# Kernel optimization log

Measured on AMD Instinct MI355X. Metric: run time of the kernel, lower is better.

## Reference

```python
import jax, jax.numpy as jnp
import numpy as np

N_NODES = 6000
DEG = 16
N_EDGES = N_NODES * DEG
D_MODEL = 256
D_MSG = 64
D_FF = 4 * D_MODEL
N_LAYERS = 3
N_SPECIES = 108
RBF_BINS = D_MODEL
RBF_VMIN, RBF_VMAX = 0.0, 8.0


def setup_inputs():
    key = jax.random.key(0)
    ks = jax.random.split(key, 16)
    rng = np.random.default_rng(0)
    # graph: each node i has DEG in-edges (dst block-structured), random sources
    atomic_number = jnp.asarray(rng.integers(1, N_SPECIES, N_NODES), dtype=jnp.int32)
    dst = np.repeat(np.arange(N_NODES), DEG)
    src = rng.integers(0, N_NODES, N_EDGES)
    # angle graph t: nodes = edges of g; edges = all ordered pairs of in-edges sharing dst
    pq = np.array([(p, q) for p in range(DEG) for q in range(DEG) if p != q], dtype=np.int64)
    off = (np.arange(N_NODES) * DEG)[:, None]
    t_src = (off + pq[:, 0][None, :]).reshape(-1)
    t_dst = (off + pq[:, 1][None, :]).reshape(-1)
    r = jax.random.normal(ks[0], (N_EDGES, 3), dtype=jnp.float32) * 2.0  # bond vectors, |r|~3A
    s_dm = 1.0 / np.sqrt(D_MODEL)
    s_dmsg = 1.0 / np.sqrt(D_MSG)
    s_ff = 1.0 / np.sqrt(D_FF)
    return {
        'r': r,
        'atomic_number': atomic_number,
        'src': jnp.asarray(src, dtype=jnp.int32),
        'dst': jnp.asarray(dst, dtype=jnp.int32),
        't_src': jnp.asarray(t_src, dtype=jnp.int32),
        't_dst': jnp.asarray(t_dst, dtype=jnp.int32),
        'emb': jax.random.normal(ks[1], (N_SPECIES, D_MODEL), dtype=jnp.float32),
        'Wsrc': jax.random.normal(ks[2], (N_LAYERS, D_MSG, D_MODEL), dtype=jnp.float32) * s_dm,
        'bsrc': jnp.zeros((N_LAYERS, D_MSG), jnp.float32),
        'Wdst': jax.random.normal(ks[3], (N_LAYERS, D_MSG, D_MODEL), dtype=jnp.float32) * s_dm,
        'bdst': jnp.zeros((N_LAYERS, D_MSG), jnp.float32),
        'Wedge': jax.random.normal(ks[4], (N_LAYERS, D_MSG, D_MODEL), dtype=jnp.float32) * s_dm,
        'bedge': jnp.zeros((N_LAYERS, D_MSG), jnp.float32),
        'attn': jax.random.normal(ks[5], (N_LAYERS, D_MSG), dtype=jnp.float32) * s_dmsg,
        'W1': jax.random.normal(ks[6], (N_LAYERS, D_FF, D_MSG), dtype=jnp.float32) * s_dmsg,
        'b1': jnp.zeros((N_LAYERS, D_FF), jnp.float32),
        'W2': jax.random.normal(ks[7], (N_LAYERS, D_MODEL, D_FF), dtype=jnp.float32) * s_ff,
        'b2': jnp.zeros((N_LAYERS, D_MODEL), jnp.float32),
        'Wfc': jax.random.normal(ks[8], (1, D_MODEL), dtype=jnp.float32) * s_dm,
        'bfc': jnp.zeros((1,), jnp.float32),
    }


def _segment_softmax(logits, seg, num):
    m = jax.ops.segment_max(logits, seg, num_segments=num)
    ex = jnp.exp(logits - m[seg])
    z = jax.ops.segment_sum(ex, seg, num_segments=num)
    return ex / z[seg]


def reference(r, atomic_number, src, dst, t_src, t_dst, emb, Wsrc, bsrc, Wdst, bdst,
              Wedge, bedge, attn, W1, b1, W2, b2, Wfc, bfc):
    x = emb[atomic_number]                                   # [N, d_model]
    d = jnp.linalg.norm(r, axis=1)                           # [E]
    centers = jnp.linspace(RBF_VMIN, RBF_VMAX, RBF_BINS, dtype=r.dtype)
    gamma = 1.0 / (centers[1] - centers[0])
    y = jnp.exp(-gamma * (d[:, None] - centers[None, :]) ** 2)  # [E, d_model]
    rhat = r / d[:, None]
    # cos angle between edge pairs (sign of -r cancels in u_dot_v)
    cos_jik = jnp.clip(jnp.sum(rhat[t_src] * rhat[t_dst], axis=1), -1.0 + 1e-6, 1.0 - 1e-6)
    nch = jnp.arange(D_MSG, dtype=r.dtype)
    z_jik = jnp.cos(nch[None, :] * jnp.arccos(cos_jik)[:, None])  # Chebyshev T_k(cos) [T, 64]
    for l in range(N_LAYERS):
        xj = x @ Wsrc[l].T + bsrc[l]                          # [N, 64]
        xi = x @ Wdst[l].T + bdst[l]
        xij = xj[src] + xi[dst] + (y @ Wedge[l].T + bedge[l])  # [E, 64]
        e_jik = jax.nn.silu(z_jik + xij[t_src] + xij[t_dst])   # [T, 64]
        logits = e_jik @ attn[l]                               # [T]
        a = _segment_softmax(logits, t_dst, N_EDGES)           # edge_softmax over angle graph
        ft = jax.ops.segment_sum(a[:, None] * xij[t_src], t_dst, num_segments=N_EDGES)  # [E, 64]
        xn = jax.ops.segment_sum(ft, dst, num_segments=N_NODES)  # scatter to nodes [N, 64]
        x = jax.nn.silu(xn @ W1[l].T + b1[l]) @ W2[l].T + b2[l]  # FFN -> [N, d_model]
    atomwise = x @ Wfc.T + bfc                                  # [N, 1]
    return jnp.squeeze(jnp.mean(atomwise, axis=0))              # AvgPooling (eV/atom)


if __name__ == '__main__':
    out = reference(**setup_inputs())
    print(out)
```

## Files before the change

### kernel.cpp

```cpp
#include <hip/hip_runtime.h>

#define N_NODES 6000
#define DEG_    16
#define N_EDGES (N_NODES*DEG_)
#define D_MODEL 256
#define D_MSG   64
#define D_FF    1024

typedef __bf16 bf16x8 __attribute__((ext_vector_type(8)));
typedef float floatx4 __attribute__((ext_vector_type(4)));

__device__ __forceinline__ float silu_f(float v) {
    return v * __builtin_amdgcn_rcpf(1.0f + __expf(-v));
}
__device__ __forceinline__ float b2f(unsigned short u) {
    union { unsigned int i; float f; } v; v.i = ((unsigned int)u) << 16; return v.f;
}
__device__ __forceinline__ unsigned short f2b(float f) {
    union { float f; unsigned int i; } v; v.f = f;
    unsigned int r = (v.i + 0x7FFFu + ((v.i >> 16) & 1u)) >> 16;
    return (unsigned short)r;
}

#define WSRC_OFF 0
#define WDST_OFF 49152
#define WEDGE_OFF 98304
#define W1_OFF 147456
#define W2_OFF 344064
#define WTOTAL 1130496
#define CVT4_BLOCKS (WTOTAL/4/256)
#define EMB4_BLOCKS (N_NODES*D_MODEL/4/256)
#define GEOM_BLOCKS (N_EDGES/256)
#define WCOMB_BLOCKS 256
#define WFC2_BLOCKS 4
#define WPACKE_BLOCKS 24
#define WPACK1_BLOCKS 64
__global__ __launch_bounds__(256) void prep_kernel(
    const float* __restrict__ Wsrc, const float* __restrict__ bsrc,
    const float* __restrict__ Wdst, const float* __restrict__ bdst,
    const float* __restrict__ Wedge, const float* __restrict__ W1,
    const float* __restrict__ W2, const float* __restrict__ b2,
    const float* __restrict__ Wfc, const float* __restrict__ bfc,
    unsigned short* __restrict__ wbf_out,
    const int* __restrict__ an, const float* __restrict__ emb,
    unsigned short* __restrict__ x,
    const float* __restrict__ r, float* __restrict__ d, float* __restrict__ rhat,
    unsigned short* __restrict__ wcomb,
    float* __restrict__ bcomb,
    float* __restrict__ wfc2,
    unsigned short* __restrict__ wedgep,
    unsigned short* __restrict__ w1p,
    float* __restrict__ out) {
    int b = blockIdx.x;
    int t = threadIdx.x;
    if (b < CVT4_BLOCKS) {
        int i = (b*256 + t) * 4;
        const float* sp;
        if      (i < WDST_OFF)  sp = Wsrc + i;
        else if (i < WEDGE_OFF) sp = Wdst + (i - WDST_OFF);
        else if (i < W1_OFF)    sp = Wedge + (i - WEDGE_OFF);
        else if (i < W2_OFF)    sp = W1 + (i - W1_OFF);
        else                    sp = W2 + (i - W2_OFF);
        float4 v = *(const float4*)sp;
        *(ushort4*)(wbf_out + i) = make_ushort4(f2b(v.x), f2b(v.y), f2b(v.z), f2b(v.w));
    } else if (b < CVT4_BLOCKS + EMB4_BLOCKS) {
        int i4 = (b - CVT4_BLOCKS)*256 + t;
        int node = i4 >> 6, c4 = i4 & 63;
        float4 v = *(const float4*)(emb + (size_t)an[node]*D_MODEL + c4*4);
        *(ushort4*)(x + (size_t)node*D_MODEL + c4*4) =
            make_ushort4(f2b(v.x), f2b(v.y), f2b(v.z), f2b(v.w));
    } else if (b < CVT4_BLOCKS + EMB4_BLOCKS + GEOM_BLOCKS) {
        int e = (b - CVT4_BLOCKS - EMB4_BLOCKS)*256 + t;
        float xx = r[e*3+0], yy = r[e*3+1], zz = r[e*3+2];
        float n = sqrtf(xx*xx + yy*yy + zz*zz);
        d[e] = n;
        float inv = 1.0f / n;
        *(float4*)(rhat + (size_t)e*4) = make_float4(xx*inv, yy*inv, zz*inv, 0.f);
    } else if (b < CVT4_BLOCKS + EMB4_BLOCKS + GEOM_BLOCKS + WCOMB_BLOCKS) {
        int wb = b - (CVT4_BLOCKS + EMB4_BLOCKS + GEOM_BLOCKS);
        int lp  = 1 + (wb >> 7);
        int row = wb & 127;
        const float* wmrow = (row < 64) ? (Wsrc + (size_t)lp*16384 + row*256)
                                        : (Wdst + (size_t)lp*16384 + (row-64)*256);
        const float* W2f = W2 + (size_t)(lp-1)*262144;
        float a0 = 0.f, a1 = 0.f, a2 = 0.f, a3 = 0.f;
        int c0 = t*4;
        #pragma unroll 4
        for (int c = 0; c < 256; ++c) {
            float wm = wmrow[c];
            float4 w2v = *(const float4*)(W2f + (size_t)c*1024 + c0);
            a0 = fmaf(wm, w2v.x, a0);
            a1 = fmaf(wm, w2v.y, a1);
            a2 = fmaf(wm, w2v.z, a2);
            a3 = fmaf(wm, w2v.w, a3);
        }
        int fc = t >> 4, j = (t >> 3) & 1, lq = (t >> 1) & 3, cpos = (t & 1) * 4;
        int wv = row >> 5, ns = (row >> 4) & 1, lr = row & 15;
        int lane = lq*16 + lr;
        *(ushort4*)(wcomb + (size_t)(lp-1)*131072
                    + (size_t)fc*8192 + wv*2048 + ns*1024 + j*512 + lane*8 + cpos) =
            make_ushort4(f2b(a0), f2b(a1), f2b(a2), f2b(a3));
    } else if (b < CVT4_BLOCKS + EMB4_BLOCKS + GEOM_BLOCKS + WCOMB_BLOCKS + WFC2_BLOCKS) {
        int wb = b - (CVT4_BLOCKS + EMB4_BLOCKS + GEOM_BLOCKS + WCOMB_BLOCKS);
        int c = wb*256 + t;
        const float* W2f = W2 + 2*262144;
        float acc = 0.f;
        for (int k = 0; k < 256; ++k) acc += Wfc[k] * W2f[(size_t)k*1024 + c];
        wfc2[c] = acc;
    } else if (b < CVT4_BLOCKS + EMB4_BLOCKS + GEOM_BLOCKS + WCOMB_BLOCKS + WFC2_BLOCKS + WPACKE_BLOCKS) {
        int wb = b - (CVT4_BLOCKS + EMB4_BLOCKS + GEOM_BLOCKS + WCOMB_BLOCKS + WFC2_BLOCKS);
        int i = wb*256 + t;
        int lane = i & 63, ks = (i >> 6) & 7, rem = i >> 9;
        int ns = rem % 3, w = rem / 3;
        int row = 48*w + ns*16 + (lane & 15);
        int col = ks*32 + (lane >> 4)*8;
        const float* sp = Wedge + (size_t)row*256 + col;
        float4 v0 = *(const float4*)sp;
        float4 v1 = *(const float4*)(sp + 4);
        unsigned short h[8] = { f2b(v0.x), f2b(v0.y), f2b(v0.z), f2b(v0.w),
                                f2b(v1.x), f2b(v1.y), f2b(v1.z), f2b(v1.w) };
        *(uint4*)(wedgep + (size_t)i*8) = *(uint4*)h;
    } else if (b < CVT4_BLOCKS + EMB4_BLOCKS + GEOM_BLOCKS + WCOMB_BLOCKS + WFC2_BLOCKS + WPACKE_BLOCKS + WPACK1_BLOCKS) {
        int wb = b - (CVT4_BLOCKS + EMB4_BLOCKS + GEOM_BLOCKS + WCOMB_BLOCKS + WFC2_BLOCKS + WPACKE_BLOCKS);
        int i2 = wb*256 + t;
        int lp = i2 >> 13;
        int e = i2 & 8191;
        int lane = e & 63, j = (e >> 6) & 1, wv = (e >> 7) & 3, f = e >> 9;
        int row = f*64 + wv*16 + (lane & 15);
        int col = j*32 + (lane >> 4)*8;
        const float* sp = W1 + (size_t)lp*65536 + (size_t)row*64 + col;
        float4 v0 = *(const float4*)sp;
        float4 v1 = *(const float4*)(sp + 4);
        unsigned short h[8] = { f2b(v0.x), f2b(v0.y), f2b(v0.z), f2b(v0.w),
                                f2b(v1.x), f2b(v1.y), f2b(v1.z), f2b(v1.w) };
        *(uint4*)(w1p + (size_t)i2*8) = *(uint4*)h;
    } else {
        int lp = 1 + (t >> 7);
        int row = t & 127;
        const float* b2l = b2 + (lp-1)*256;
        const float* wmrow = (row < 64) ? (Wsrc + (size_t)lp*16384 + row*256)
                                        : (Wdst + (size_t)lp*16384 + (row-64)*256);
        float acc = 0.f;
        for (int c = 0; c < 256; ++c) acc += wmrow[c] * b2l[c];
        acc += (row < 64) ? bsrc[lp*64 + row] : bdst[lp*64 + (row-64)];
        bcomb[(lp-1)*128 + row] = acc;
        if (t == 0) {
            float bo = 0.f;
            const float* b23 = b2 + 2*256;
            for (int c = 0; c < 256; ++c) bo += Wfc[c] * b23[c];
            out[0] = bo + bfc[0];
        }
    }
}

#define EPITCH 264
#define APITCH 40
#define MCP 72
__global__ __launch_bounds__(256) void eplg_kernel(
    const unsigned short* __restrict__ Bwp,
    const float* __restrict__ bias,
    const float* __restrict__ dvec,
    unsigned short* __restrict__ C,
    const unsigned short* __restrict__ A,
    const unsigned short* __restrict__ B1g,
    const unsigned short* __restrict__ B2g,
    const float* __restrict__ bias1,
    const float* __restrict__ bias2,
    unsigned short* __restrict__ Cg) {
    __shared__ __align__(16) unsigned short sm[64*EPITCH];
    const int t = threadIdx.x;
    const int w = t >> 6, lane = t & 63, lr = lane & 15, lq = lane >> 4;

    if (blockIdx.x < 1500) {
        unsigned short* As = sm;
        const int m0 = blockIdx.x * 64;
        const int arow = t >> 2, achk = t & 3;

        float dv = dvec[m0 + arow];
        const float gamma = 31.875f;
        const float step  = 8.0f / 255.0f;
        #pragma unroll
        for (int c32 = 0; c32 < 8; ++c32) {
            int kb = c32*32 + achk*8;
            unsigned short h[8];
            #pragma unroll
            for (int j = 0; j < 8; ++j) {
                float tt = dv - (float)(kb+j)*step;
                h[j] = f2b(__expf(-gamma*tt*tt));
            }
            *(uint4*)(&As[arow*EPITCH + kb]) = *(uint4*)h;
        }
        __syncthreads();

        const unsigned short* Bp = Bwp + (size_t)w*12288 + lane*8;

        floatx4 acc[4][3] = {};
        uint4 pb[3];
        #pragma unroll
        for (int ns = 0; ns < 3; ++ns)
            pb[ns] = *(const uint4*)(Bp + ns*4096);

        for (int k0 = 0; k0 < 256; k0 += 32) {
            int ks = k0 >> 5;
            uint4 cb[3];
            cb[0] = pb[0]; cb[1] = pb[1]; cb[2] = pb[2];
            if (k0 + 32 < 256) {
                #pragma unroll
                for (int ns = 0; ns < 3; ++ns)
                    pb[ns] = *(const uint4*)(Bp + ns*4096 + (ks+1)*512);
            }
            bf16x8 af[4];
            #pragma unroll
            for (int mi = 0; mi < 4; ++mi)
                af[mi] = *(const bf16x8*)(&As[(mi*16 + lr)*EPITCH + k0 + lq*8]);
            #pragma unroll
            for (int mi = 0; mi < 4; ++mi) {
                #pragma unroll
                for (int ns = 0; ns < 3; ++ns)
                    acc[mi][ns] = __builtin_amdgcn_mfma_f32_16x16x32_bf16(
                        af[mi], *(const bf16x8*)&cb[ns], acc[mi][ns], 0, 0, 0);
            }
        }

        #pragma unroll
        for (int ns = 0; ns < 3; ++ns) {
            int bc = 48*w + ns*16 + lr;
            float bv = bias[bc];
            #pragma unroll
            for (int mi = 0; mi < 4; ++mi) {
                #pragma unroll
                for (int rg = 0; rg < 4; ++rg) {
                    int row = m0 + mi*16 + lq*4 + rg;
                    C[(size_t)row*192 + bc] = f2b(acc[mi][ns][rg] + bv);
                }
            }
        }
        return;
    }
    {
        unsigned short* As = sm;
        unsigned short* Bs = sm + 2560;
        unsigned short* Cs = sm;
        const int bid2 = blockIdx.x - 1500;
        const int bx = bid2 & 1;
        const int m0 = (bid2 >> 1) * 64;
        const unsigned short* B = bx ? B2g : B1g;
        const float* biasl = bx ? bias2 : bias1;
        const int n0 = bx * 64;
        const int K = 256, M = N_NODES, lda = 256, ldb = 256, ldc = 128;

        const int arow = t >> 2, achk = t & 3;

        floatx4 acc[4] = {};
        uint4 pa, pb;
        {
            int gm = m0 + arow;
            pa = (gm < M) ? *(const uint4*)(A + (size_t)gm*lda + achk*8) : make_uint4(0,0,0,0);
        }
        pb = *(const uint4*)(B + (size_t)arow*ldb + achk*8);

        for (int k0 = 0; k0 < K; k0 += 32) {
            *(uint4*)(&As[arow*APITCH + achk*8]) = pa;
            *(uint4*)(&Bs[arow*APITCH + achk*8]) = pb;
            __syncthreads();
            if (k0 + 32 < K) {
                int kn = k0 + 32;
                int gm = m0 + arow;
                pa = (gm < M) ? *(const uint4*)(A + (size_t)gm*lda + kn + achk*8) : make_uint4(0,0,0,0);
                pb = *(const uint4*)(B + (size_t)arow*ldb + kn + achk*8);
            }
            bf16x8 af, bfr[4];
            af = *(const bf16x8*)(&As[(w*16 + lr)*APITCH + lq*8]);
            #pragma unroll
            for (int ns = 0; ns < 4; ++ns)
                bfr[ns] = *(const bf16x8*)(&Bs[(ns*16 + lr)*APITCH + lq*8]);
            #pragma unroll
            for (int ns = 0; ns < 4; ++ns)
                acc[ns] = __builtin_amdgcn_mfma_f32_16x16x32_bf16(af, bfr[ns], acc[ns], 0,0,0);
            __syncthreads();
        }
        #pragma unroll
        for (int ns = 0; ns < 4; ++ns) {
            int bc = ns*16 + lr;
            float bv = biasl[bc];
            #pragma unroll
            for (int rg = 0; rg < 4; ++rg) {
                int lrow = w*16 + lq*4 + rg;
                Cs[lrow*MCP + bc] = f2b(acc[ns][rg] + bv);
            }
        }
        __syncthreads();
        #pragma unroll
        for (int it = 0; it < 2; ++it) {
            int i = t + it*256;
            int row = i >> 3, c8 = i & 7;
            int gm = m0 + row;
            if (gm < M)
                *(uint4*)(Cg + (size_t)gm*ldc + n0 + c8*8) = *(const uint4*)(Cs + row*MCP + c8*8);
        }
    }
}

template<int ACT, int DUALB>
__global__ __launch_bounds__(256) void mgemm(
    const unsigned short* __restrict__ A, int lda,
    const unsigned short* __restrict__ B1, const unsigned short* __restrict__ B2, int ldb,
    const float* __restrict__ bias1, const float* __restrict__ bias2,
    unsigned short* __restrict__ C, int ldc, int M, int K) {
    __shared__ __align__(16) unsigned short sm[5120];
    unsigned short* As = sm;
    unsigned short* Bs = sm + 2560;
    unsigned short* Cs = sm;
    const int t = threadIdx.x;
    const int w = t >> 6;
    const int lane = t & 63;
    const int lr = lane & 15;
    const int lq = lane >> 4;
    const int n0 = blockIdx.x * 64;
    const int m0 = blockIdx.y * 64;
    const unsigned short* B = B1;
    const float* bias = bias1;
    if (DUALB && blockIdx.x == 1) { B = B2; bias = bias2; }
    const unsigned short* Brow = DUALB ? B : (B + (size_t)n0*ldb);

    const int arow = t >> 2, achk = t & 3;

    floatx4 acc[4] = {};
    uint4 pa, pb;
    {
        int gm = m0 + arow;
        pa = (gm < M) ? *(const uint4*)(A + (size_t)gm*lda + achk*8) : make_uint4(0,0,0,0);
    }
    pb = *(const uint4*)(Brow + (size_t)arow*ldb + achk*8);

    for (int k0 = 0; k0 < K; k0 += 32) {
        *(uint4*)(&As[arow*APITCH + achk*8]) = pa;
        *(uint4*)(&Bs[arow*APITCH + achk*8]) = pb;
        __syncthreads();
        if (k0 + 32 < K) {
            int kn = k0 + 32;
            int gm = m0 + arow;
            pa = (gm < M) ? *(const uint4*)(A + (size_t)gm*lda + kn + achk*8) : make_uint4(0,0,0,0);
            pb = *(const uint4*)(Brow + (size_t)arow*ldb + kn + achk*8);
        }
        bf16x8 af, bfr[4];
        af = *(const bf16x8*)(&As[(w*16 + lr)*APITCH + lq*8]);
        #pragma unroll
        for (int ns = 0; ns < 4; ++ns)
            bfr[ns] = *(const bf16x8*)(&Bs[(ns*16 + lr)*APITCH + lq*8]);
        #pragma unroll
        for (int ns = 0; ns < 4; ++ns)
            acc[ns] = __builtin_amdgcn_mfma_f32_16x16x32_bf16(af, bfr[ns], acc[ns], 0,0,0);
        __syncthreads();
    }
    if (ACT == 2) {
        float partial = 0.f;
        #pragma unroll
        for (int ns = 0; ns < 4; ++ns) {
            int bc = ns*16 + lr;
            float bv = bias[n0 + bc];
            float wv = bias2[n0 + bc];
            #pragma unroll
            for (int rg = 0; rg < 4; ++rg) {
                int gm = m0 + w*16 + lq*4 + rg;
                float v = silu_f(acc[ns][rg] + bv);
                if (gm < M) partial += v * wv;
            }
        }
        float* red = (float*)sm;
        red[t] = partial;
        __syncthreads();
        for (int off = 128; off > 0; off >>= 1) {
            if (t < off) red[t] += red[t+off];
            __syncthreads();
        }
        if (t == 0) atomicAdd((float*)C, red[0] * (1.0f/(float)N_NODES));
        return;
    }
    #pragma unroll
    for (int ns = 0; ns < 4; ++ns) {
        int bc = ns*16 + lr;
        float bv = bias[DUALB ? bc : (n0 + bc)];
        #pragma unroll
        for (int rg = 0; rg < 4; ++rg) {
            int lrow = w*16 + lq*4 + rg;
            float v = acc[ns][rg] + bv;
            if (ACT) v = silu_f(v);
            Cs[lrow*MCP + bc] = f2b(v);
        }
    }
    __syncthreads();
    #pragma unroll
    for (int it = 0; it < 2; ++it) {
        int i = t + it*256;
        int row = i >> 3, c8 = i & 7;
        int gm = m0 + row;
        if (gm < M)
            *(uint4*)(C + (size_t)gm*ldc + n0 + c8*8) = *(const uint4*)(Cs + row*MCP + c8*8);
    }
}

#define HP 72
#define CP2 136
__global__ __launch_bounds__(256) void ffw_kernel(
    const unsigned short* __restrict__ XN,
    const unsigned short* __restrict__ W1p,
    const float* __restrict__ b1l,
    const unsigned short* __restrict__ WCp,
    const float* __restrict__ bcl,
    unsigned short* __restrict__ XO,
    int M) {
    __shared__ __align__(16) unsigned short s_h[16*HP];
    __shared__ __align__(16) unsigned short s_c[16*CP2];
    const int t = threadIdx.x;
    const int wv = t >> 6, lane = t & 63, lr = lane & 15, lq = lane >> 4;
    const int m0 = blockIdx.x * 16;

    int ga = m0 + lr;
    bool aok = ga < M;
    uint4 a0 = aok ? *(const uint4*)(XN + (size_t)ga*64 + lq*8) : make_uint4(0,0,0,0);
    uint4 a1 = aok ? *(const uint4*)(XN + (size_t)ga*64 + 32 + lq*8) : make_uint4(0,0,0,0);

    floatx4 acc2[2] = {};

    const unsigned short* W1b = W1p + (size_t)wv*1024 + lane*8;
    const unsigned short* WCb = WCp + (size_t)wv*2048 + lane*8;

    uint4 pb1[2], pb2[4];
    pb1[0] = *(const uint4*)(W1b);
    pb1[1] = *(const uint4*)(W1b + 512);
    pb2[0] = *(const uint4*)(WCb);
    pb2[1] = *(const uint4*)(WCb + 512);
    pb2[2] = *(const uint4*)(WCb + 1024);
    pb2[3] = *(const uint4*)(WCb + 1536);

    for (int f = 0; f < 16; ++f) {
        uint4 cb1_0 = pb1[0], cb1_1 = pb1[1];
        uint4 cb2_0 = pb2[0], cb2_1 = pb2[1], cb2_2 = pb2[2], cb2_3 = pb2[3];
        float bv1 = b1l[f*64 + wv*16 + lr];
        if (f < 15) {
            const unsigned short* n1 = W1b + (f+1)*4096;
            const unsigned short* n2 = WCb + (f+1)*8192;
            pb1[0] = *(const uint4*)(n1);
            pb1[1] = *(const uint4*)(n1 + 512);
            pb2[0] = *(const uint4*)(n2);
            pb2[1] = *(const uint4*)(n2 + 512);
            pb2[2] = *(const uint4*)(n2 + 1024);
            pb2[3] = *(const uint4*)(n2 + 1536);
        }
        floatx4 hacc = {};
        hacc = __builtin_amdgcn_mfma_f32_16x16x32_bf16(
            *(const bf16x8*)&a0, *(const bf16x8*)&cb1_0, hacc, 0,0,0);
        hacc = __builtin_amdgcn_mfma_f32_16x16x32_bf16(
            *(const bf16x8*)&a1, *(const bf16x8*)&cb1_1, hacc, 0,0,0);
        {
            int col = wv*16 + lr;
            #pragma unroll
            for (int rg = 0; rg < 4; ++rg) {
                int row = lq*4 + rg;
                s_h[row*HP + col] = f2b(silu_f(hacc[rg] + bv1));
            }
        }
        __syncthreads();
        bf16x8 ha0 = *(const bf16x8*)(&s_h[lr*HP + lq*8]);
        bf16x8 ha1 = *(const bf16x8*)(&s_h[lr*HP + 32 + lq*8]);
        acc2[0] = __builtin_amdgcn_mfma_f32_16x16x32_bf16(ha0, *(const bf16x8*)&cb2_0, acc2[0], 0,0,0);
        acc2[0] = __builtin_amdgcn_mfma_f32_16x16x32_bf16(ha1, *(const bf16x8*)&cb2_1, acc2[0], 0,0,0);
        acc2[1] = __builtin_amdgcn_mfma_f32_16x16x32_bf16(ha0, *(const bf16x8*)&cb2_2, acc2[1], 0,0,0);
        acc2[1] = __builtin_amdgcn_mfma_f32_16x16x32_bf16(ha1, *(const bf16x8*)&cb2_3, acc2[1], 0,0,0);
        __syncthreads();
    }

    #pragma unroll
    for (int ns = 0; ns < 2; ++ns) {
        int col = wv*32 + ns*16 + lr;
        float bv = bcl[col];
        #pragma unroll
        for (int rg = 0; rg < 4; ++rg) {
            int row = lq*4 + rg;
            s_c[row*CP2 + col] = f2b(acc2[ns][rg] + bv);
        }
    }
    __syncthreads();
    {
        int row = t >> 4, c8 = t & 15;
        int gm = m0 + row;
        if (gm < M)
            *(uint4*)(XO + (size_t)gm*128 + c8*8) = *(const uint4*)(s_c + row*CP2 + c8*8);
    }
}

__global__ __launch_bounds__(256) void angle_kernel(
    const unsigned short* __restrict__ xjxi,
    const unsigned short* __restrict__ eproj,
    const float* __restrict__ rhat,
    const int*   __restrict__ src,
    const float* __restrict__ attn,
    unsigned short* __restrict__ xn) {
    __shared__ __align__(16) float s_xij[2][16][68];
    __shared__ float s_rhat[2][16][4];
    __shared__ float s_logit[2][16][17];
    __shared__ float s_e[2][16][17];
    __shared__ float s_m[2][16], s_zi[2][16];
    __shared__ float s_w[2][16];
    const int t = threadIdx.x;
    const int h = t >> 7, tt = t & 127;
    const int node = blockIdx.x*2 + h;

    if (tt < 16) {
        float4 rv = *(const float4*)(rhat + (size_t)(node*DEG_ + tt)*4);
        s_rhat[h][tt][0] = rv.x; s_rhat[h][tt][1] = rv.y; s_rhat[h][tt][2] = rv.z; s_rhat[h][tt][3] = 0.f;
        s_e[h][tt][tt] = 0.f;
    }
    {
        int p = tt >> 3, c8 = tt & 7;
        int e = node*DEG_ + p;
        int se = src[e];
        uint4 aj = *(const uint4*)(xjxi + (size_t)se*128 + c8*8);
        uint4 ai = *(const uint4*)(xjxi + (size_t)node*128 + 64 + c8*8);
        uint4 ae = *(const uint4*)(eproj + (size_t)e*192 + c8*8);
        const unsigned short* pj = (const unsigned short*)&aj;
        const unsigned short* pi = (const unsigned short*)&ai;
        const unsigned short* pe = (const unsigned short*)&ae;
        #pragma unroll
        for (int j = 0; j < 8; ++j)
            s_xij[h][p][c8*8 + j] = b2f(pj[j]) + b2f(pi[j]) + b2f(pe[j]);
    }
    __syncthreads();
    int pp = 0, qq = 0;
    float lg = 0.f;
    if (tt < 120) {
        pp = (int)((1.0f + sqrtf(8.0f*(float)tt + 1.0f)) * 0.5f);
        qq = tt - ((pp*(pp-1)) >> 1);
        float c = s_rhat[h][pp][0]*s_rhat[h][qq][0] + s_rhat[h][pp][1]*s_rhat[h][qq][1]
                + s_rhat[h][pp][2]*s_rhat[h][qq][2];
        c = fminf(fmaxf(c, -0.999999f), 0.999999f);
        float c2  = 2.0f * c;
        float tk0 = 1.0f;
        float tk1 = c;
        float acc = 0.f;
        const float* xp = &s_xij[h][pp][0];
        const float* xq = &s_xij[h][qq][0];
        #pragma unroll
        for (int k0 = 0; k0 < 64; k0 += 4) {
            float4 xp4 = *(const float4*)(xp + k0);
            float4 xq4 = *(const float4*)(xq + k0);
            float a0 = attn[k0+0], a1 = attn[k0+1], a2 = attn[k0+2], a3 = attn[k0+3];
            float v0 = tk0 + xp4.x + xq4.x;
            acc = fmaf(a0, silu_f(v0), acc);
            { float tn2 = c2*tk1 - tk0; tk0 = tk1; tk1 = tn2; }
            float v1 = tk0 + xp4.y + xq4.y;
            acc = fmaf(a1, silu_f(v1), acc);
            { float tn2 = c2*tk1 - tk0; tk0 = tk1; tk1 = tn2; }
            float v2 = tk0 + xp4.z + xq4.z;
            acc = fmaf(a2, silu_f(v2), acc);
            { float tn2 = c2*tk1 - tk0; tk0 = tk1; tk1 = tn2; }
            float v3 = tk0 + xp4.w + xq4.w;
            acc = fmaf(a3, silu_f(v3), acc);
            { float tn2 = c2*tk1 - tk0; tk0 = tk1; tk1 = tn2; }
        }
        lg = acc;
        s_logit[h][pp][qq] = acc;
        s_logit[h][qq][pp] = acc;
    }
    __syncthreads();
    if (tt < 16) {
        int q = tt;
        float mx = -1e30f;
        #pragma unroll
        for (int p = 0; p < 16; ++p) if (p != q) mx = fmaxf(mx, s_logit[h][p][q]);
        s_m[h][q] = mx;
    }
    __syncthreads();
    if (tt < 120) {
        s_e[h][pp][qq] = __expf(lg - s_m[h][qq]);
        s_e[h][qq][pp] = __expf(lg - s_m[h][pp]);
    }
    __syncthreads();
    if (tt < 16) {
        int q = tt;
        float z = 0.f;
        #pragma unroll
        for (int p = 0; p < 16; ++p) z += s_e[h][p][q];
        s_zi[h][q] = __builtin_amdgcn_rcpf(z);
    }
    __syncthreads();
    if (tt < 16) {
        int p = tt;
        float sw = 0.f;
        #pragma unroll
        for (int q = 0; q < 16; ++q) sw += s_e[h][p][q] * s_zi[h][q];
        s_w[h][p] = sw;
    }
    __syncthreads();
    if (tt < 64) {
        float acc = 0.f;
        #pragma unroll
        for (int p = 0; p < 16; ++p) acc += s_w[h][p] * s_xij[h][p][tt];
        xn[(size_t)node*64 + tt] = f2b(acc);
    }
}

extern "C" void kernel_launch(void* const* d_in, const int* in_sizes, int n_in,
                              void* d_out, int out_size, void* d_ws, size_t ws_size,
                              hipStream_t stream) {
    (void)in_sizes; (void)n_in; (void)out_size; (void)ws_size;
    const float* r    = (const float*)d_in[0];
    const int*   an   = (const int*)  d_in[1];
    const int*   src  = (const int*)  d_in[2];
    const float* emb  = (const float*)d_in[6];
    const float* Wsrc = (const float*)d_in[7];
    const float* bsrc = (const float*)d_in[8];
    const float* Wdst = (const float*)d_in[9];
    const float* bdst = (const float*)d_in[10];
    const float* Wedge= (const float*)d_in[11];
    const float* bedge= (const float*)d_in[12];
    const float* attn = (const float*)d_in[13];
    const float* W1   = (const float*)d_in[14];
    const float* b1   = (const float*)d_in[15];
    const float* W2   = (const float*)d_in[16];
    const float* b2   = (const float*)d_in[17];
    const float* Wfc  = (const float*)d_in[18];
    const float* bfc  = (const float*)d_in[19];

    char* ws = (char*)d_ws;
    float* d_d              = (float*)(ws);
    float* d_rhat           = (float*)(ws + 384000);
    unsigned short* wbf     = (unsigned short*)(ws + 1920000);
    unsigned short* d_x     = (unsigned short*)(ws + 4180992);
    unsigned short* d_xjxi  = (unsigned short*)(ws + 7252992);
    unsigned short* d_eproj = (unsigned short*)(ws + 8788992);
    unsigned short* d_xn    = (unsigned short*)(ws + 45652992);
    unsigned short* d_wcomb = (unsigned short*)(ws + 46420992);
    float* d_bcomb          = (float*)(ws + 46945280);
    float* d_wfc2           = (float*)(ws + 46946304);
    unsigned short* d_wedgep= (unsigned short*)(ws + 46950400);
    unsigned short* d_w1p   = (unsigned short*)(ws + 47048704);
    float* out = (float*)d_out;

    unsigned short* wsrc_bf  = wbf + WSRC_OFF;
    unsigned short* wdst_bf  = wbf + WDST_OFF;
    unsigned short* w1_bf    = wbf + W1_OFF;

    prep_kernel<<<CVT4_BLOCKS + EMB4_BLOCKS + GEOM_BLOCKS + WCOMB_BLOCKS + WFC2_BLOCKS
                  + WPACKE_BLOCKS + WPACK1_BLOCKS + 1, 256, 0, stream>>>(
        Wsrc, bsrc, Wdst, bdst, Wedge, W1, W2, b2, Wfc, bfc,
        wbf, an, emb, d_x, r, d_d, d_rhat, d_wcomb, d_bcomb, d_wfc2,
        d_wedgep, d_w1p, out);

    eplg_kernel<<<1500 + 188, 256, 0, stream>>>(
        d_wedgep, bedge, d_d, d_eproj,
        d_x, wsrc_bf, wdst_bf, bsrc, bdst, d_xjxi);

    angle_kernel<<<N_NODES/2, 256, 0, stream>>>(
        d_xjxi, d_eproj, d_rhat, src, attn, d_xn);
    ffw_kernel<<<375, 256, 0, stream>>>(
        d_xn, d_w1p, b1, d_wcomb, d_bcomb, d_xjxi, N_NODES);

    angle_kernel<<<N_NODES/2, 256, 0, stream>>>(
        d_xjxi, d_eproj + 64, d_rhat, src, attn + 64, d_xn);
    ffw_kernel<<<375, 256, 0, stream>>>(
        d_xn, d_w1p + 65536, b1 + 1024, d_wcomb + 131072, d_bcomb + 128, d_xjxi, N_NODES);

    angle_kernel<<<N_NODES/2, 256, 0, stream>>>(
        d_xjxi, d_eproj + 128, d_rhat, src, attn + 128, d_xn);
    mgemm<2,0><<<dim3(16,94), 256, 0, stream>>>(
        d_xn, 64, w1_bf + 131072, (const unsigned short*)nullptr, 64,
        b1 + 2048, d_wfc2, (unsigned short*)out, 0, N_NODES, 64);
}
```

Baseline: 253.6 us.

## Split angle work per node across pairs, add fused final FFN kernel, trim prep conversion

The angle kernel now handles one node per block. Each angle pair is split across two threads, one per half of the 64 channels. The second thread jumps straight to Chebyshev T32/T33 by doubling, and the two partial logits are combined with a lane shuffle. The final layer's generic mgemm is replaced by a dedicated ffa_kernel that keeps the A tile in registers, streams packed W1 and reduces silu(h)·wfc2 directly into the output. The prep kernel stops converting Wedge/W1/W2 to bf16 and instead packs all three layers' W1 into the packed layout. The pair split improves parallelism in the logit phase but doubles the block count and leaves many threads idle during the softmax stages.

```diff
diff --git a/kernel.cpp b/kernel.cpp
--- a/kernel.cpp
+++ b/kernel.cpp
@@ -24,17 +24,14 @@
 
 #define WSRC_OFF 0
 #define WDST_OFF 49152
-#define WEDGE_OFF 98304
-#define W1_OFF 147456
-#define W2_OFF 344064
-#define WTOTAL 1130496
-#define CVT4_BLOCKS (WTOTAL/4/256)
+#define WCVT_TOTAL 98304
+#define CVT4_BLOCKS (WCVT_TOTAL/4/256)
 #define EMB4_BLOCKS (N_NODES*D_MODEL/4/256)
 #define GEOM_BLOCKS (N_EDGES/256)
 #define WCOMB_BLOCKS 256
 #define WFC2_BLOCKS 4
 #define WPACKE_BLOCKS 24
-#define WPACK1_BLOCKS 64
+#define WPACK1_BLOCKS 96
 __global__ __launch_bounds__(256) void prep_kernel(
     const float* __restrict__ Wsrc, const float* __restrict__ bsrc,
     const float* __restrict__ Wdst, const float* __restrict__ bdst,
@@ -55,12 +52,7 @@
     int t = threadIdx.x;
     if (b < CVT4_BLOCKS) {
         int i = (b*256 + t) * 4;
-        const float* sp;
-        if      (i < WDST_OFF)  sp = Wsrc + i;
-        else if (i < WEDGE_OFF) sp = Wdst + (i - WDST_OFF);
-        else if (i < W1_OFF)    sp = Wedge + (i - WEDGE_OFF);
-        else if (i < W2_OFF)    sp = W1 + (i - W1_OFF);
-        else                    sp = W2 + (i - W2_OFF);
+        const float* sp = (i < WDST_OFF) ? (Wsrc + i) : (Wdst + (i - WDST_OFF));
         float4 v = *(const float4*)sp;
         *(ushort4*)(wbf_out + i) = make_ushort4(f2b(v.x), f2b(v.y), f2b(v.z), f2b(v.w));
     } else if (b < CVT4_BLOCKS + EMB4_BLOCKS) {
@@ -301,105 +293,6 @@
     }
 }
 
-template<int ACT, int DUALB>
-__global__ __launch_bounds__(256) void mgemm(
-    const unsigned short* __restrict__ A, int lda,
-    const unsigned short* __restrict__ B1, const unsigned short* __restrict__ B2, int ldb,
-    const float* __restrict__ bias1, const float* __restrict__ bias2,
-    unsigned short* __restrict__ C, int ldc, int M, int K) {
-    __shared__ __align__(16) unsigned short sm[5120];
-    unsigned short* As = sm;
-    unsigned short* Bs = sm + 2560;
-    unsigned short* Cs = sm;
-    const int t = threadIdx.x;
-    const int w = t >> 6;
-    const int lane = t & 63;
-    const int lr = lane & 15;
-    const int lq = lane >> 4;
-    const int n0 = blockIdx.x * 64;
-    const int m0 = blockIdx.y * 64;
-    const unsigned short* B = B1;
-    const float* bias = bias1;
-    if (DUALB && blockIdx.x == 1) { B = B2; bias = bias2; }
-    const unsigned short* Brow = DUALB ? B : (B + (size_t)n0*ldb);
-
-    const int arow = t >> 2, achk = t & 3;
-
-    floatx4 acc[4] = {};
-    uint4 pa, pb;
-    {
-        int gm = m0 + arow;
-        pa = (gm < M) ? *(const uint4*)(A + (size_t)gm*lda + achk*8) : make_uint4(0,0,0,0);
-    }
-    pb = *(const uint4*)(Brow + (size_t)arow*ldb + achk*8);
-
-    for (int k0 = 0; k0 < K; k0 += 32) {
-        *(uint4*)(&As[arow*APITCH + achk*8]) = pa;
-        *(uint4*)(&Bs[arow*APITCH + achk*8]) = pb;
-        __syncthreads();
-        if (k0 + 32 < K) {
-            int kn = k0 + 32;
-            int gm = m0 + arow;
-            pa = (gm < M) ? *(const uint4*)(A + (size_t)gm*lda + kn + achk*8) : make_uint4(0,0,0,0);
-            pb = *(const uint4*)(Brow + (size_t)arow*ldb + kn + achk*8);
-        }
-        bf16x8 af, bfr[4];
-        af = *(const bf16x8*)(&As[(w*16 + lr)*APITCH + lq*8]);
-        #pragma unroll
-        for (int ns = 0; ns < 4; ++ns)
-            bfr[ns] = *(const bf16x8*)(&Bs[(ns*16 + lr)*APITCH + lq*8]);
-        #pragma unroll
-        for (int ns = 0; ns < 4; ++ns)
-            acc[ns] = __builtin_amdgcn_mfma_f32_16x16x32_bf16(af, bfr[ns], acc[ns], 0,0,0);
-        __syncthreads();
-    }
-    if (ACT == 2) {
-        float partial = 0.f;
-        #pragma unroll
-        for (int ns = 0; ns < 4; ++ns) {
-            int bc = ns*16 + lr;
-            float bv = bias[n0 + bc];
-            float wv = bias2[n0 + bc];
-            #pragma unroll
-            for (int rg = 0; rg < 4; ++rg) {
-                int gm = m0 + w*16 + lq*4 + rg;
-                float v = silu_f(acc[ns][rg] + bv);
-                if (gm < M) partial += v * wv;
-            }
-        }
-        float* red = (float*)sm;
-        red[t] = partial;
-        __syncthreads();
-        for (int off = 128; off > 0; off >>= 1) {
-            if (t < off) red[t] += red[t+off];
-            __syncthreads();
-        }
-        if (t == 0) atomicAdd((float*)C, red[0] * (1.0f/(float)N_NODES));
-        return;
-    }
-    #pragma unroll
-    for (int ns = 0; ns < 4; ++ns) {
-        int bc = ns*16 + lr;
-        float bv = bias[DUALB ? bc : (n0 + bc)];
-        #pragma unroll
-        for (int rg = 0; rg < 4; ++rg) {
-            int lrow = w*16 + lq*4 + rg;
-            float v = acc[ns][rg] + bv;
-            if (ACT) v = silu_f(v);
-            Cs[lrow*MCP + bc] = f2b(v);
-        }
-    }
-    __syncthreads();
-    #pragma unroll
-    for (int it = 0; it < 2; ++it) {
-        int i = t + it*256;
-        int row = i >> 3, c8 = i & 7;
-        int gm = m0 + row;
-        if (gm < M)
-            *(uint4*)(C + (size_t)gm*ldc + n0 + c8*8) = *(const uint4*)(Cs + row*MCP + c8*8);
-    }
-}
-
 #define HP 72
 #define CP2 136
 __global__ __launch_bounds__(256) void ffw_kernel(
@@ -490,6 +383,55 @@
     }
 }
 
+__global__ __launch_bounds__(256) void ffa_kernel(
+    const unsigned short* __restrict__ XN,
+    const unsigned short* __restrict__ W1p,
+    const float* __restrict__ b1l,
+    const float* __restrict__ wfc2,
+    float* __restrict__ out, int M) {
+    __shared__ float red[256];
+    const int t = threadIdx.x;
+    const int wv = t >> 6, lane = t & 63, lr = lane & 15, lq = lane >> 4;
+    const int m0 = blockIdx.x * 16;
+
+    int ga = m0 + lr;
+    bool aok = ga < M;
+    uint4 a0 = aok ? *(const uint4*)(XN + (size_t)ga*64 + lq*8) : make_uint4(0,0,0,0);
+    uint4 a1 = aok ? *(const uint4*)(XN + (size_t)ga*64 + 32 + lq*8) : make_uint4(0,0,0,0);
+
+    const unsigned short* W1b = W1p + (size_t)wv*1024 + lane*8;
+    uint4 pb0 = *(const uint4*)(W1b);
+    uint4 pb1 = *(const uint4*)(W1b + 512);
+
+    float partial = 0.f;
+    for (int f = 0; f < 16; ++f) {
+        uint4 c0 = pb0, c1 = pb1;
+        if (f < 15) {
+            pb0 = *(const uint4*)(W1b + (f+1)*4096);
+            pb1 = *(const uint4*)(W1b + (f+1)*4096 + 512);
+        }
+        floatx4 hacc = {};
+        hacc = __builtin_amdgcn_mfma_f32_16x16x32_bf16(
+            *(const bf16x8*)&a0, *(const bf16x8*)&c0, hacc, 0,0,0);
+        hacc = __builtin_amdgcn_mfma_f32_16x16x32_bf16(
+            *(const bf16x8*)&a1, *(const bf16x8*)&c1, hacc, 0,0,0);
+        float bv1 = b1l[f*64 + wv*16 + lr];
+        float wvv = wfc2[f*64 + wv*16 + lr];
+        #pragma unroll
+        for (int rg = 0; rg < 4; ++rg) {
+            int gm = m0 + lq*4 + rg;
+            if (gm < M) partial += silu_f(hacc[rg] + bv1) * wvv;
+        }
+    }
+    red[t] = partial;
+    __syncthreads();
+    for (int off = 128; off > 0; off >>= 1) {
+        if (t < off) red[t] += red[t+off];
+        __syncthreads();
+    }
+    if (t == 0) atomicAdd(out, red[0] * (1.0f/(float)N_NODES));
+}
+
 __global__ __launch_bounds__(256) void angle_kernel(
     const unsigned short* __restrict__ xjxi,
     const unsigned short* __restrict__ eproj,
@@ -497,55 +439,68 @@
     const int*   __restrict__ src,
     const float* __restrict__ attn,
     unsigned short* __restrict__ xn) {
-    __shared__ __align__(16) float s_xij[2][16][68];
-    __shared__ float s_rhat[2][16][4];
-    __shared__ float s_logit[2][16][17];
-    __shared__ float s_e[2][16][17];
-    __shared__ float s_m[2][16], s_zi[2][16];
-    __shared__ float s_w[2][16];
-    const int t = threadIdx.x;
-    const int h = t >> 7, tt = t & 127;
-    const int node = blockIdx.x*2 + h;
+    __shared__ __align__(16) float s_xij[16][68];
+    __shared__ float s_rhat[16][4];
+    __shared__ float s_logit[16][17];
+    __shared__ float s_e[16][17];
+    __shared__ float s_m[16], s_zi[16];
+    __shared__ float s_w[16];
+    const int tt = threadIdx.x;
+    const int node = blockIdx.x;
 
     if (tt < 16) {
         float4 rv = *(const float4*)(rhat + (size_t)(node*DEG_ + tt)*4);
-        s_rhat[h][tt][0] = rv.x; s_rhat[h][tt][1] = rv.y; s_rhat[h][tt][2] = rv.z; s_rhat[h][tt][3] = 0.f;
-        s_e[h][tt][tt] = 0.f;
+        s_rhat[tt][0] = rv.x; s_rhat[tt][1] = rv.y; s_rhat[tt][2] = rv.z; s_rhat[tt][3] = 0.f;
+        s_e[tt][tt] = 0.f;
     }
     {
-        int p = tt >> 3, c8 = tt & 7;
+        int p = tt >> 4, c4 = tt & 15;
         int e = node*DEG_ + p;
         int se = src[e];
-        uint4 aj = *(const uint4*)(xjxi + (size_t)se*128 + c8*8);
-        uint4 ai = *(const uint4*)(xjxi + (size_t)node*128 + 64 + c8*8);
-        uint4 ae = *(const uint4*)(eproj + (size_t)e*192 + c8*8);
-        const unsigned short* pj = (const unsigned short*)&aj;
-        const unsigned short* pi = (const unsigned short*)&ai;
-        const unsigned short* pe = (const unsigned short*)&ae;
-        #pragma unroll
-        for (int j = 0; j < 8; ++j)
-            s_xij[h][p][c8*8 + j] = b2f(pj[j]) + b2f(pi[j]) + b2f(pe[j]);
+        ushort4 aj = *(const ushort4*)(xjxi + (size_t)se*128 + c4*4);
+        ushort4 ai = *(const ushort4*)(xjxi + (size_t)node*128 + 64 + c4*4);
+        ushort4 ae = *(const ushort4*)(eproj + (size_t)e*192 + c4*4);
+        s_xij[p][c4*4+0] = b2f(aj.x) + b2f(ai.x) + b2f(ae.x);
+        s_xij[p][c4*4+1] = b2f(aj.y) + b2f(ai.y) + b2f(ae.y);
+        s_xij[p][c4*4+2] = b2f(aj.z) + b2f(ai.z) + b2f(ae.z);
+        s_xij[p][c4*4+3] = b2f(aj.w) + b2f(ai.w) + b2f(ae.w);
     }
     __syncthreads();
     int pp = 0, qq = 0;
     float lg = 0.f;
-    if (tt < 120) {
-        pp = (int)((1.0f + sqrtf(8.0f*(float)tt + 1.0f)) * 0.5f);
-        qq = tt - ((pp*(pp-1)) >> 1);
-        float c = s_rhat[h][pp][0]*s_rhat[h][qq][0] + s_rhat[h][pp][1]*s_rhat[h][qq][1]
-                + s_rhat[h][pp][2]*s_rhat[h][qq][2];
+    if (tt < 240) {
+        int pair = tt >> 1, half = tt & 1;
+        pp = (int)((1.0f + sqrtf(8.0f*(float)pair + 1.0f)) * 0.5f);
+        qq = pair - ((pp*(pp-1)) >> 1);
+        float c = s_rhat[pp][0]*s_rhat[qq][0] + s_rhat[pp][1]*s_rhat[qq][1]
+                + s_rhat[pp][2]*s_rhat[qq][2];
         c = fminf(fmaxf(c, -0.999999f), 0.999999f);
-        float c2  = 2.0f * c;
-        float tk0 = 1.0f;
-        float tk1 = c;
+        float c2 = 2.0f * c;
+        float tk0, tk1;
+        if (half) {
+            float T2  = fmaf(c2, c, -1.0f);
+            float T3  = fmaf(2.0f*T2,  c,   -c);
+            float T4  = fmaf(2.0f*T2,  T2,  -1.0f);
+            float T7  = fmaf(2.0f*T4,  T3,  -c);
+            float T8  = fmaf(2.0f*T4,  T4,  -1.0f);
+            float T15 = fmaf(2.0f*T8,  T7,  -c);
+            float T16 = fmaf(2.0f*T8,  T8,  -1.0f);
+            float T31 = fmaf(2.0f*T16, T15, -c);
+            float T32 = fmaf(2.0f*T16, T16, -1.0f);
+            float T33 = fmaf(2.0f*T32, c,   -T31);
+            tk0 = T32; tk1 = T33;
+        } else {
+            tk0 = 1.0f; tk1 = c;
+        }
+        const float* xp = &s_xij[pp][0] + half*32;
+        const float* xq = &s_xij[qq][0] + half*32;
+        const float* at = attn + half*32;
         float acc = 0.f;
-        const float* xp = &s_xij[h][pp][0];
-        const float* xq = &s_xij[h][qq][0];
-        #pragma unroll
-        for (int k0 = 0; k0 < 64; k0 += 4) {
+        #pragma unroll
+        for (int k0 = 0; k0 < 32; k0 += 4) {
             float4 xp4 = *(const float4*)(xp + k0);
             float4 xq4 = *(const float4*)(xq + k0);
-            float a0 = attn[k0+0], a1 = attn[k0+1], a2 = attn[k0+2], a3 = attn[k0+3];
+            float a0 = at[k0+0], a1 = at[k0+1], a2 = at[k0+2], a3 = at[k0+3];
             float v0 = tk0 + xp4.x + xq4.x;
             acc = fmaf(a0, silu_f(v0), acc);
             { float tn2 = c2*tk1 - tk0; tk0 = tk1; tk1 = tn2; }
@@ -560,43 +515,49 @@
             { float tn2 = c2*tk1 - tk0; tk0 = tk1; tk1 = tn2; }
         }
         lg = acc;
-        s_logit[h][pp][qq] = acc;
-        s_logit[h][qq][pp] = acc;
+    }
+    lg += __shfl_xor(lg, 1);
+    if (tt < 240 && (tt & 1) == 0) {
+        s_logit[pp][qq] = lg;
+        s_logit[qq][pp] = lg;
     }
     __syncthreads();
     if (tt < 16) {
         int q = tt;
         float mx = -1e30f;
         #pragma unroll
-        for (int p = 0; p < 16; ++p) if (p != q) mx = fmaxf(mx, s_logit[h][p][q]);
-        s_m[h][q] = mx;
+        for (int p = 0; p < 16; ++p) if (p != q) mx = fmaxf(mx, s_logit[p][q]);
+        s_m[q] = mx;
     }
     __syncthreads();
     if (tt < 120) {
-        s_e[h][pp][qq] = __expf(lg - s_m[h][qq]);
-        s_e[h][qq][pp] = __expf(lg - s_m[h][pp]);
+        int p2 = (int)((1.0f + sqrtf(8.0f*(float)tt + 1.0f)) * 0.5f);
+        int q2 = tt - ((p2*(p2-1)) >> 1);
+        float l = s_logit[p2][q2];
+        s_e[p2][q2] = __expf(l - s_m[q2]);
+        s_e[q2][p2] = __expf(l - s_m[p2]);
     }
     __syncthreads();
     if (tt < 16) {
         int q = tt;
         float z = 0.f;
         #pragma unroll
-        for (int p = 0; p < 16; ++p) z += s_e[h][p][q];
-        s_zi[h][q] = __builtin_amdgcn_rcpf(z);
+        for (int p = 0; p < 16; ++p) z += s_e[p][q];
+        s_zi[q] = __builtin_amdgcn_rcpf(z);
     }
     __syncthreads();
     if (tt < 16) {
         int p = tt;
         float sw = 0.f;
         #pragma unroll
-        for (int q = 0; q < 16; ++q) sw += s_e[h][p][q] * s_zi[h][q];
-        s_w[h][p] = sw;
+        for (int q = 0; q < 16; ++q) sw += s_e[p][q] * s_zi[q];
+        s_w[p] = sw;
     }
     __syncthreads();
     if (tt < 64) {
         float acc = 0.f;
         #pragma unroll
-        for (int p = 0; p < 16; ++p) acc += s_w[h][p] * s_xij[h][p][tt];
+        for (int p = 0; p < 16; ++p) acc += s_w[p] * s_xij[p][tt];
         xn[(size_t)node*64 + tt] = f2b(acc);
     }
 }
@@ -640,7 +601,6 @@
 
     unsigned short* wsrc_bf  = wbf + WSRC_OFF;
     unsigned short* wdst_bf  = wbf + WDST_OFF;
-    unsigned short* w1_bf    = wbf + W1_OFF;
 
     prep_kernel<<<CVT4_BLOCKS + EMB4_BLOCKS + GEOM_BLOCKS + WCOMB_BLOCKS + WFC2_BLOCKS
                   + WPACKE_BLOCKS + WPACK1_BLOCKS + 1, 256, 0, stream>>>(
@@ -652,19 +612,18 @@
         d_wedgep, bedge, d_d, d_eproj,
         d_x, wsrc_bf, wdst_bf, bsrc, bdst, d_xjxi);
 
-    angle_kernel<<<N_NODES/2, 256, 0, stream>>>(
+    angle_kernel<<<N_NODES, 256, 0, stream>>>(
         d_xjxi, d_eproj, d_rhat, src, attn, d_xn);
     ffw_kernel<<<375, 256, 0, stream>>>(
         d_xn, d_w1p, b1, d_wcomb, d_bcomb, d_xjxi, N_NODES);
 
-    angle_kernel<<<N_NODES/2, 256, 0, stream>>>(
+    angle_kernel<<<N_NODES, 256, 0, stream>>>(
         d_xjxi, d_eproj + 64, d_rhat, src, attn + 64, d_xn);
     ffw_kernel<<<375, 256, 0, stream>>>(
         d_xn, d_w1p + 65536, b1 + 1024, d_wcomb + 131072, d_bcomb + 128, d_xjxi, N_NODES);
 
-    angle_kernel<<<N_NODES/2, 256, 0, stream>>>(
+    angle_kernel<<<N_NODES, 256, 0, stream>>>(
         d_xjxi, d_eproj + 128, d_rhat, src, attn + 128, d_xn);
-    mgemm<2,0><<<dim3(16,94), 256, 0, stream>>>(
-        d_xn, 64, w1_bf + 131072, (const unsigned short*)nullptr, 64,
-        b1 + 2048, d_wfc2, (unsigned short*)out, 0, N_NODES, 64);
-}
+    ffa_kernel<<<375, 256, 0, stream>>>(
+        d_xn, d_w1p + 131072, b1 + 2048, d_wfc2, out, N_NODES);
+}
```

Result: no change. 251.3 us (-0.9%).
